# Kernel tuning notes

Measured on AMD Instinct MI355X. Metric: run time of the kernel, lower is better.

## Reference

```python
import jax, jax.numpy as jnp
import numpy as np

B = 65536
IN_F = 1024
OUT_F = 1024
N_ACT = 4  # len(activation_functions): tanh, sin, relu, sigmoid (cyclic over columns)


def setup_inputs() -> dict:
    key = jax.random.key(0)
    k1, k2 = jax.random.split(key)
    x = jax.random.normal(k1, (B, IN_F), dtype=jnp.float32)
    # xavier_uniform for weight [out, in]
    limit = float(np.sqrt(6.0 / (IN_F + OUT_F)))
    W = jax.random.uniform(k2, (OUT_F, IN_F), dtype=jnp.float32, minval=-limit, maxval=limit)
    b = jnp.zeros((OUT_F,), dtype=jnp.float32)
    return {"input": x, "W": W, "b": b}


def _apply_cyclic_acts(y):
    # column i gets activation (i % N_ACT); OUT_F % N_ACT == 0 so reshape to groups
    Bb, O = y.shape
    yg = y.reshape(Bb, O // N_ACT, N_ACT)
    out = jnp.stack([
        jnp.tanh(yg[..., 0]),
        jnp.sin(yg[..., 1]),
        jax.nn.relu(yg[..., 2]),
        jax.nn.sigmoid(yg[..., 3]),
    ], axis=-1)
    return out.reshape(Bb, O)


def reference(input, W, b) -> jnp.ndarray:
    y = jnp.einsum('bi,oi->bo', input, W) + b  # F.linear
    return _apply_cyclic_acts(y)
```

## Files before the change

### kernel.cpp

```cpp
#include <hip/hip_runtime.h>

constexpr int B_ROWS = 65536;
constexpr int IN_F   = 1024;
constexpr int OUT_F  = 1024;

constexpr int BDIM = 256;
constexpr int BM = 128, BN = 128, BK = 32;

typedef __bf16 bf16x8 __attribute__((ext_vector_type(8)));
typedef float  f32x4  __attribute__((ext_vector_type(4)));

__device__ __forceinline__ bf16x8 cvt8(f32x4 u0, f32x4 u1) {
    bf16x8 v;
    v[0] = (__bf16)u0[0]; v[1] = (__bf16)u0[1]; v[2] = (__bf16)u0[2]; v[3] = (__bf16)u0[3];
    v[4] = (__bf16)u1[0]; v[5] = (__bf16)u1[1]; v[6] = (__bf16)u1[2]; v[7] = (__bf16)u1[3];
    return v;
}

__device__ __forceinline__ void glds16(const __bf16* g, unsigned char* l) {
    __builtin_amdgcn_global_load_lds(
        (const __attribute__((address_space(1))) unsigned int*)(const void*)g,
        (__attribute__((address_space(3))) unsigned int*)(void*)l,
        16, 0, 0);
}

#define BAR_CNT() asm volatile("s_waitcnt vmcnt(4) lgkmcnt(0)\n\ts_barrier" ::: "memory")
#define BAR_ALL() asm volatile("s_waitcnt vmcnt(0) lgkmcnt(0)\n\ts_barrier" ::: "memory")

__global__ __launch_bounds__(256)
void w_to_bf16(const float* __restrict__ W, __bf16* __restrict__ Wb) {
    const int i = (blockIdx.x * 256 + threadIdx.x) * 8;
    f32x4 a = *(const f32x4*)(W + i);
    f32x4 b = *(const f32x4*)(W + i + 4);
    *(bf16x8*)(Wb + i) = cvt8(a, b);
}

__global__ __launch_bounds__(BDIM, 4)
void fused_linear_act(const float* __restrict__ X,
                      const __bf16* __restrict__ Wb,
                      const float* __restrict__ bias,
                      float* __restrict__ O)
{
    __shared__ __attribute__((aligned(16))) unsigned char lds[2 * 16384];

    const int bx  = blockIdx.x;
    const int xcd = bx & 7;
    const int idx = bx >> 3;
    const int nt  = idx & 7;
    const int mt  = xcd + 8 * (idx >> 3);
    const int m0 = mt * BM;
    const int n0 = nt * BN;

    const int tid  = threadIdx.x;
    const int lane = tid & 63;
    const int wave = tid >> 6;
    const int wm = (wave >> 1) * 64;
    const int wn = (wave & 1) * 64;
    const int lrow = lane & 15;
    const int quad = lane >> 4;

    const int srow = tid >> 2;
    const int sseg = tid & 3;

    f32x4 acc[4][4];
    #pragma unroll
    for (int i = 0; i < 4; ++i)
        #pragma unroll
        for (int j = 0; j < 4; ++j)
            acc[i][j] = (f32x4){0.f, 0.f, 0.f, 0.f};

    const float* xa = X + (size_t)(m0 + srow) * IN_F + sseg * 8;
    const float* xb = xa + (size_t)64 * IN_F;

    const __bf16* wsrc0 = Wb + (size_t)(n0 + 16 * wave + lrow) * IN_F + quad * 8;
    const __bf16* wsrc1 = wsrc0 + (size_t)64 * IN_F;
    unsigned char* ldsB0 = lds + 8192 + wave * 1024;
    unsigned char* ldsB1 = ldsB0 + 4096;

    unsigned char* wr = &lds[((srow >> 4) * 64 + sseg * 16 + (srow & 15)) * 16];
    const unsigned char* rdA = &lds[(wm >> 4) * 1024 + lane * 16];
    const unsigned char* rdB = &lds[8192 + (wn >> 4) * 1024 + lane * 16];

    f32x4 A00 = *(const f32x4*)(xa);
    f32x4 A01 = *(const f32x4*)(xa + 4);
    f32x4 A10 = *(const f32x4*)(xb);
    f32x4 A11 = *(const f32x4*)(xb + 4);
    glds16(wsrc0, ldsB0);
    glds16(wsrc1, ldsB1);
    __builtin_amdgcn_sched_barrier(0);

    int koffA = 0;
    int koffB = 0;

    auto stageA = [&](int buf) {
        unsigned char* w = wr + buf * 16384;
        *(bf16x8*)(w +    0) = cvt8(A00, A01);
        *(bf16x8*)(w + 4096) = cvt8(A10, A11);
        koffA = (koffA + BK) & (IN_F - 1);
        A00 = *(const f32x4*)(xa + koffA); A01 = *(const f32x4*)(xa + koffA + 4);
        A10 = *(const f32x4*)(xb + koffA); A11 = *(const f32x4*)(xb + koffA + 4);
    };
    auto stageB = [&](int buf) {
        koffB += BK;
        glds16(wsrc0 + koffB, ldsB0 + buf * 16384);
        glds16(wsrc1 + koffB, ldsB1 + buf * 16384);
        __builtin_amdgcn_sched_barrier(0);
    };
    auto compute = [&](int buf) {
        const unsigned char* ra = rdA + buf * 16384;
        const unsigned char* rb = rdB + buf * 16384;
        bf16x8 af[4], bfr[4];
        #pragma unroll
        for (int t = 0; t < 4; ++t) af[t]  = *(const bf16x8*)(ra + t * 1024);
        #pragma unroll
        for (int t = 0; t < 4; ++t) bfr[t] = *(const bf16x8*)(rb + t * 1024);
        #pragma unroll
        for (int i = 0; i < 4; ++i)
            #pragma unroll
            for (int j = 0; j < 4; ++j)
                acc[i][j] = __builtin_amdgcn_mfma_f32_16x16x32_bf16(af[i], bfr[j], acc[i][j], 0, 0, 0);
    };

    #pragma unroll 1
    for (int it = 0; it < IN_F / BK - 2; it += 2) {
        stageA(0); BAR_CNT(); stageB(1); compute(0);
        stageA(1); BAR_CNT(); stageB(0); compute(1);
    }
    stageA(0); BAR_CNT(); stageB(1); compute(0);
    stageA(1); BAR_ALL(); compute(1);

    const int s = lane & 3;
    const float kmul = (s == 0) ? -2.f : -1.f;
    const float aa   = (s == 0) ?  2.f :  1.f;
    const float cc   = (s == 0) ? -1.f :  0.f;
    const bool  is_sin  = (s == 1);
    const bool  is_relu = (s == 2);

    #pragma unroll
    for (int j = 0; j < 4; ++j) {
        const int gc = n0 + wn + j * 16 + lrow;
        const float bv = bias[gc];
        #pragma unroll
        for (int i = 0; i < 4; ++i) {
            const int gr0 = m0 + wm + i * 16 + quad * 4;
            float* op = O + (size_t)gr0 * OUT_F + gc;
            #pragma unroll
            for (int r = 0; r < 4; ++r) {
                const float y = acc[i][j][r] + bv;
                const float e = __expf(kmul * y);
                const float g = fmaf(aa, __builtin_amdgcn_rcpf(1.f + e), cc);
                const float sv = __sinf(y);
                const float rv = fmaxf(y, 0.f);
                const float res = is_sin ? sv : (is_relu ? rv : g);
                op[(size_t)r * OUT_F] = res;
            }
        }
    }
}

extern "C" void kernel_launch(void* const* d_in, const int* in_sizes, int n_in,
                              void* d_out, int out_size, void* d_ws, size_t ws_size,
                              hipStream_t stream) {
    const float* X = (const float*)d_in[0];
    const float* W = (const float*)d_in[1];
    const float* b = (const float*)d_in[2];
    float* O = (float*)d_out;
    __bf16* Wb = (__bf16*)d_ws;

    w_to_bf16<<<(OUT_F * IN_F) / (256 * 8), 256, 0, stream>>>(W, Wb);

    const int grid = (B_ROWS / BM) * (OUT_F / BN);
    fused_linear_act<<<grid, BDIM, 0, stream>>>(X, Wb, b, O);
}
```

Before: 654.8 us.

## Pre-convert activations to bf16 and triple-buffer async LDS loads for both operands

```diff
diff --git a/kernel.cpp b/kernel.cpp
--- a/kernel.cpp
+++ b/kernel.cpp
@@ -24,24 +24,27 @@
         16, 0, 0);
 }
 
-#define BAR_CNT() asm volatile("s_waitcnt vmcnt(4) lgkmcnt(0)\n\ts_barrier" ::: "memory")
-#define BAR_ALL() asm volatile("s_waitcnt vmcnt(0) lgkmcnt(0)\n\ts_barrier" ::: "memory")
+#define BARC() asm volatile("s_waitcnt vmcnt(4) lgkmcnt(0)\n\ts_barrier" ::: "memory")
+#define BAR0() asm volatile("s_waitcnt vmcnt(0) lgkmcnt(0)\n\ts_barrier" ::: "memory")
 
 __global__ __launch_bounds__(256)
-void w_to_bf16(const float* __restrict__ W, __bf16* __restrict__ Wb) {
-    const int i = (blockIdx.x * 256 + threadIdx.x) * 8;
-    f32x4 a = *(const f32x4*)(W + i);
-    f32x4 b = *(const f32x4*)(W + i + 4);
-    *(bf16x8*)(Wb + i) = cvt8(a, b);
-}
-
-__global__ __launch_bounds__(BDIM, 4)
-void fused_linear_act(const float* __restrict__ X,
+void cvt_bf16(const float* __restrict__ in, __bf16* __restrict__ out) {
+    const size_t i = ((size_t)blockIdx.x * 256 + threadIdx.x) * 16;
+    f32x4 a0 = *(const f32x4*)(in + i);
+    f32x4 a1 = *(const f32x4*)(in + i + 4);
+    f32x4 a2 = *(const f32x4*)(in + i + 8);
+    f32x4 a3 = *(const f32x4*)(in + i + 12);
+    *(bf16x8*)(out + i)     = cvt8(a0, a1);
+    *(bf16x8*)(out + i + 8) = cvt8(a2, a3);
+}
+
+__global__ __launch_bounds__(BDIM, 3)
+void fused_linear_act(const __bf16* __restrict__ Xb,
                       const __bf16* __restrict__ Wb,
                       const float* __restrict__ bias,
                       float* __restrict__ O)
 {
-    __shared__ __attribute__((aligned(16))) unsigned char lds[2 * 16384];
+    __shared__ __attribute__((aligned(16))) unsigned char lds[3 * 16384];
 
     const int bx  = blockIdx.x;
     const int xcd = bx & 7;
@@ -59,6 +62,116 @@
     const int lrow = lane & 15;
     const int quad = lane >> 4;
 
+    f32x4 acc[4][4];
+    #pragma unroll
+    for (int i = 0; i < 4; ++i)
+        #pragma unroll
+        for (int j = 0; j < 4; ++j)
+            acc[i][j] = (f32x4){0.f, 0.f, 0.f, 0.f};
+
+    const __bf16* asrc0 = Xb + (size_t)(m0 + 16 * wave + lrow) * IN_F + quad * 8;
+    const __bf16* asrc1 = asrc0 + (size_t)64 * IN_F;
+    const __bf16* bsrc0 = Wb + (size_t)(n0 + 16 * wave + lrow) * IN_F + quad * 8;
+    const __bf16* bsrc1 = bsrc0 + (size_t)64 * IN_F;
+    const int wlds = wave * 1024;
+
+    unsigned char* const buf0 = lds;
+    unsigned char* const buf1 = lds + 16384;
+    unsigned char* const buf2 = lds + 32768;
+
+    const int rdAoff = (wm >> 4) * 1024 + lane * 16;
+    const int rdBoff = 8192 + (wn >> 4) * 1024 + lane * 16;
+
+    auto stage = [&](int koff, unsigned char* base) {
+        glds16(asrc0 + koff, base + wlds);
+        glds16(asrc1 + koff, base + wlds + 4096);
+        glds16(bsrc0 + koff, base + 8192 + wlds);
+        glds16(bsrc1 + koff, base + 8192 + wlds + 4096);
+    };
+    auto compute = [&](const unsigned char* base) {
+        const unsigned char* ra = base + rdAoff;
+        const unsigned char* rb = base + rdBoff;
+        bf16x8 af[4], bfr[4];
+        #pragma unroll
+        for (int t = 0; t < 4; ++t) af[t]  = *(const bf16x8*)(ra + t * 1024);
+        #pragma unroll
+        for (int t = 0; t < 4; ++t) bfr[t] = *(const bf16x8*)(rb + t * 1024);
+        #pragma unroll
+        for (int i = 0; i < 4; ++i)
+            #pragma unroll
+            for (int j = 0; j < 4; ++j)
+                acc[i][j] = __builtin_amdgcn_mfma_f32_16x16x32_bf16(af[i], bfr[j], acc[i][j], 0, 0, 0);
+    };
+
+    stage(0,  buf0);
+    stage(32, buf1);
+
+    int koff = 64;
+    #pragma unroll 1
+    for (int it = 0; it < 10; ++it) {
+        BARC(); stage(koff, buf2); compute(buf0); koff += 32;
+        BARC(); stage(koff, buf0); compute(buf1); koff += 32;
+        BARC(); stage(koff, buf1); compute(buf2); koff += 32;
+    }
+    BARC(); compute(buf0);
+    BAR0(); compute(buf1);
+
+    const int s = lane & 3;
+    const float kmul = (s == 0) ? -2.f : -1.f;
+    const float aa   = (s == 0) ?  2.f :  1.f;
+    const float cc   = (s == 0) ? -1.f :  0.f;
+    const bool  is_sin  = (s == 1);
+    const bool  is_relu = (s == 2);
+
+    float bv[4];
+    #pragma unroll
+    for (int j = 0; j < 4; ++j) bv[j] = bias[n0 + wn + j * 16 + lrow];
+
+    #pragma unroll
+    for (int i = 0; i < 4; ++i) {
+        #pragma unroll
+        for (int r = 0; r < 4; ++r) {
+            const int gr = m0 + wm + i * 16 + quad * 4 + r;
+            float* op = O + (size_t)gr * OUT_F + n0 + wn + lrow;
+            #pragma unroll
+            for (int j = 0; j < 4; ++j) {
+                const float y = acc[i][j][r] + bv[j];
+                const float e = __expf(kmul * y);
+                const float g = fmaf(aa, __builtin_amdgcn_rcpf(1.f + e), cc);
+                const float sv = __sinf(y);
+                const float rv = fmaxf(y, 0.f);
+                const float res = is_sin ? sv : (is_relu ? rv : g);
+                op[j * 16] = res;
+            }
+        }
+    }
+}
+
+#define LDS_SYNC() asm volatile("s_waitcnt lgkmcnt(0)\n\ts_barrier" ::: "memory")
+#define BAR_CNT() asm volatile("s_waitcnt vmcnt(4) lgkmcnt(0)\n\ts_barrier" ::: "memory")
+#define BAR_ALL() asm volatile("s_waitcnt vmcnt(0) lgkmcnt(0)\n\ts_barrier" ::: "memory")
+
+__global__ __launch_bounds__(BDIM, 4)
+void fused_linear_act_f32a(const float* __restrict__ X,
+                           const __bf16* __restrict__ Wb,
+                           const float* __restrict__ bias,
+                           float* __restrict__ O)
+{
+    __shared__ __attribute__((aligned(16))) unsigned char lds[2 * 16384];
+    const int bx  = blockIdx.x;
+    const int xcd = bx & 7;
+    const int idx = bx >> 3;
+    const int nt  = idx & 7;
+    const int mt  = xcd + 8 * (idx >> 3);
+    const int m0 = mt * BM;
+    const int n0 = nt * BN;
+    const int tid  = threadIdx.x;
+    const int lane = tid & 63;
+    const int wave = tid >> 6;
+    const int wm = (wave >> 1) * 64;
+    const int wn = (wave & 1) * 64;
+    const int lrow = lane & 15;
+    const int quad = lane >> 4;
     const int srow = tid >> 2;
     const int sseg = tid & 3;
 
@@ -71,12 +184,10 @@
 
     const float* xa = X + (size_t)(m0 + srow) * IN_F + sseg * 8;
     const float* xb = xa + (size_t)64 * IN_F;
-
     const __bf16* wsrc0 = Wb + (size_t)(n0 + 16 * wave + lrow) * IN_F + quad * 8;
     const __bf16* wsrc1 = wsrc0 + (size_t)64 * IN_F;
     unsigned char* ldsB0 = lds + 8192 + wave * 1024;
     unsigned char* ldsB1 = ldsB0 + 4096;
-
     unsigned char* wr = &lds[((srow >> 4) * 64 + sseg * 16 + (srow & 15)) * 16];
     const unsigned char* rdA = &lds[(wm >> 4) * 1024 + lane * 16];
     const unsigned char* rdB = &lds[8192 + (wn >> 4) * 1024 + lane * 16];
@@ -89,9 +200,7 @@
     glds16(wsrc1, ldsB1);
     __builtin_amdgcn_sched_barrier(0);
 
-    int koffA = 0;
-    int koffB = 0;
-
+    int koffA = 0, koffB = 0;
     auto stageA = [&](int buf) {
         unsigned char* w = wr + buf * 16384;
         *(bf16x8*)(w +    0) = cvt8(A00, A01);
@@ -135,18 +244,17 @@
     const float cc   = (s == 0) ? -1.f :  0.f;
     const bool  is_sin  = (s == 1);
     const bool  is_relu = (s == 2);
-
     #pragma unroll
     for (int j = 0; j < 4; ++j) {
         const int gc = n0 + wn + j * 16 + lrow;
-        const float bv = bias[gc];
+        const float bvv = bias[gc];
         #pragma unroll
         for (int i = 0; i < 4; ++i) {
             const int gr0 = m0 + wm + i * 16 + quad * 4;
             float* op = O + (size_t)gr0 * OUT_F + gc;
             #pragma unroll
             for (int r = 0; r < 4; ++r) {
-                const float y = acc[i][j][r] + bv;
+                const float y = acc[i][j][r] + bvv;
                 const float e = __expf(kmul * y);
                 const float g = fmaf(aa, __builtin_amdgcn_rcpf(1.f + e), cc);
                 const float sv = __sinf(y);
@@ -165,10 +273,21 @@
     const float* W = (const float*)d_in[1];
     const float* b = (const float*)d_in[2];
     float* O = (float*)d_out;
-    __bf16* Wb = (__bf16*)d_ws;
-
-    w_to_bf16<<<(OUT_F * IN_F) / (256 * 8), 256, 0, stream>>>(W, Wb);
-
+
+    const size_t nX = (size_t)B_ROWS * IN_F;
+    const size_t nW = (size_t)OUT_F * IN_F;
+    const size_t need = (nX + nW) * sizeof(__bf16);
     const int grid = (B_ROWS / BM) * (OUT_F / BN);
-    fused_linear_act<<<grid, BDIM, 0, stream>>>(X, Wb, b, O);
-}
+
+    if (ws_size >= need) {
+        __bf16* Xb = (__bf16*)d_ws;
+        __bf16* Wb = Xb + nX;
+        cvt_bf16<<<(int)(nX / (256 * 16)), 256, 0, stream>>>(X, Xb);
+        cvt_bf16<<<(int)(nW / (256 * 16)), 256, 0, stream>>>(W, Wb);
+        fused_linear_act<<<grid, BDIM, 0, stream>>>(Xb, Wb, b, O);
+    } else {
+        __bf16* Wb = (__bf16*)d_ws;
+        cvt_bf16<<<(int)(nW / (256 * 16)), 256, 0, stream>>>(W, Wb);
+        fused_linear_act_f32a<<<grid, BDIM, 0, stream>>>(X, Wb, b, O);
+    }
+}
```

Measured after the change: 690.6 us. 1.05x slower.

## Enlarge GEMM tiles to 256x256x64 with 8 waves and interleaved LDS pipeline

Applied to the files above, without the earlier changes.

```diff
diff --git a/kernel.cpp b/kernel.cpp
--- a/kernel.cpp
+++ b/kernel.cpp
@@ -4,8 +4,8 @@
 constexpr int IN_F   = 1024;
 constexpr int OUT_F  = 1024;
 
-constexpr int BDIM = 256;
-constexpr int BM = 128, BN = 128, BK = 32;
+constexpr int BDIM = 512;
+constexpr int BM = 256, BN = 256, BK = 64;
 
 typedef __bf16 bf16x8 __attribute__((ext_vector_type(8)));
 typedef float  f32x4  __attribute__((ext_vector_type(4)));
@@ -24,110 +24,145 @@
         16, 0, 0);
 }
 
-#define BAR_CNT() asm volatile("s_waitcnt vmcnt(4) lgkmcnt(0)\n\ts_barrier" ::: "memory")
-#define BAR_ALL() asm volatile("s_waitcnt vmcnt(0) lgkmcnt(0)\n\ts_barrier" ::: "memory")
-
 __global__ __launch_bounds__(256)
 void w_to_bf16(const float* __restrict__ W, __bf16* __restrict__ Wb) {
-    const int i = (blockIdx.x * 256 + threadIdx.x) * 8;
-    f32x4 a = *(const f32x4*)(W + i);
-    f32x4 b = *(const f32x4*)(W + i + 4);
-    *(bf16x8*)(Wb + i) = cvt8(a, b);
-}
-
-__global__ __launch_bounds__(BDIM, 4)
+    const size_t i = ((size_t)blockIdx.x * 256 + threadIdx.x) * 16;
+    f32x4 a0 = *(const f32x4*)(W + i);
+    f32x4 a1 = *(const f32x4*)(W + i + 4);
+    f32x4 a2 = *(const f32x4*)(W + i + 8);
+    f32x4 a3 = *(const f32x4*)(W + i + 12);
+    *(bf16x8*)(Wb + i)     = cvt8(a0, a1);
+    *(bf16x8*)(Wb + i + 8) = cvt8(a2, a3);
+}
+
+
+__global__ __launch_bounds__(BDIM, 2)
 void fused_linear_act(const float* __restrict__ X,
                       const __bf16* __restrict__ Wb,
                       const float* __restrict__ bias,
                       float* __restrict__ O)
 {
-    __shared__ __attribute__((aligned(16))) unsigned char lds[2 * 16384];
+    __shared__ __attribute__((aligned(16))) unsigned char lds[2 * 65536];
 
     const int bx  = blockIdx.x;
     const int xcd = bx & 7;
     const int idx = bx >> 3;
-    const int nt  = idx & 7;
-    const int mt  = xcd + 8 * (idx >> 3);
+    const int nt  = idx & 3;
+    const int mt  = xcd + 8 * (idx >> 2);
     const int m0 = mt * BM;
     const int n0 = nt * BN;
 
     const int tid  = threadIdx.x;
     const int lane = tid & 63;
     const int wave = tid >> 6;
-    const int wm = (wave >> 1) * 64;
-    const int wn = (wave & 1) * 64;
+    const int wm2  = (wave >> 2) * 128;
+    const int wn2  = (wave & 3) * 64;
     const int lrow = lane & 15;
     const int quad = lane >> 4;
 
-    const int srow = tid >> 2;
-    const int sseg = tid & 3;
-
-    f32x4 acc[4][4];
+    const int arow = tid >> 1;
+    const int ah   = tid & 1;
+    const float* asrc = X + (size_t)(m0 + arow) * IN_F + ah * 32;
+    const int awr = ah * 16384 + (arow >> 4) * 1024 + (arow & 15) * 16;
+
+    const __bf16* bs0 = Wb + (size_t)(n0 + (wave & 3) * 64 + lrow) * IN_F
+                           + (wave >> 2) * 32 + quad * 8;
+    const __bf16* bs1 = bs0 + (size_t)16 * IN_F;
+    const __bf16* bs2 = bs0 + (size_t)32 * IN_F;
+    const __bf16* bs3 = bs0 + (size_t)48 * IN_F;
+    const int bdst = 32768 + (wave >> 2) * 16384 + (wave & 3) * 4096;
+
+    const int rdA = (wave >> 2) * 8192 + lane * 16;
+    const int rdB = 32768 + (wave & 3) * 4096 + lane * 16;
+
+    unsigned char* const b0 = lds;
+    unsigned char* const b1 = lds + 65536;
+
+    f32x4 acc[8][4];
     #pragma unroll
-    for (int i = 0; i < 4; ++i)
+    for (int i = 0; i < 8; ++i)
         #pragma unroll
         for (int j = 0; j < 4; ++j)
             acc[i][j] = (f32x4){0.f, 0.f, 0.f, 0.f};
 
-    const float* xa = X + (size_t)(m0 + srow) * IN_F + sseg * 8;
-    const float* xb = xa + (size_t)64 * IN_F;
-
-    const __bf16* wsrc0 = Wb + (size_t)(n0 + 16 * wave + lrow) * IN_F + quad * 8;
-    const __bf16* wsrc1 = wsrc0 + (size_t)64 * IN_F;
-    unsigned char* ldsB0 = lds + 8192 + wave * 1024;
-    unsigned char* ldsB1 = ldsB0 + 4096;
-
-    unsigned char* wr = &lds[((srow >> 4) * 64 + sseg * 16 + (srow & 15)) * 16];
-    const unsigned char* rdA = &lds[(wm >> 4) * 1024 + lane * 16];
-    const unsigned char* rdB = &lds[8192 + (wn >> 4) * 1024 + lane * 16];
-
-    f32x4 A00 = *(const f32x4*)(xa);
-    f32x4 A01 = *(const f32x4*)(xa + 4);
-    f32x4 A10 = *(const f32x4*)(xb);
-    f32x4 A11 = *(const f32x4*)(xb + 4);
-    glds16(wsrc0, ldsB0);
-    glds16(wsrc1, ldsB1);
-    __builtin_amdgcn_sched_barrier(0);
-
-    int koffA = 0;
-    int koffB = 0;
-
-    auto stageA = [&](int buf) {
-        unsigned char* w = wr + buf * 16384;
-        *(bf16x8*)(w +    0) = cvt8(A00, A01);
-        *(bf16x8*)(w + 4096) = cvt8(A10, A11);
-        koffA = (koffA + BK) & (IN_F - 1);
-        A00 = *(const f32x4*)(xa + koffA); A01 = *(const f32x4*)(xa + koffA + 4);
-        A10 = *(const f32x4*)(xb + koffA); A11 = *(const f32x4*)(xb + koffA + 4);
-    };
-    auto stageB = [&](int buf) {
-        koffB += BK;
-        glds16(wsrc0 + koffB, ldsB0 + buf * 16384);
-        glds16(wsrc1 + koffB, ldsB1 + buf * 16384);
-        __builtin_amdgcn_sched_barrier(0);
-    };
-    auto compute = [&](int buf) {
-        const unsigned char* ra = rdA + buf * 16384;
-        const unsigned char* rb = rdB + buf * 16384;
-        bf16x8 af[4], bfr[4];
-        #pragma unroll
-        for (int t = 0; t < 4; ++t) af[t]  = *(const bf16x8*)(ra + t * 1024);
-        #pragma unroll
-        for (int t = 0; t < 4; ++t) bfr[t] = *(const bf16x8*)(rb + t * 1024);
-        #pragma unroll
-        for (int i = 0; i < 4; ++i)
-            #pragma unroll
-            for (int j = 0; j < 4; ++j)
-                acc[i][j] = __builtin_amdgcn_mfma_f32_16x16x32_bf16(af[i], bfr[j], acc[i][j], 0, 0, 0);
-    };
+    f32x4 ar0, ar1, ar2, ar3, ar4, ar5, ar6, ar7;
+    bf16x8 aq0, aq1, aq2, aq3, bq0, bq1, bq2, bq3;
+
+#define ALOAD_LO(KA) do { \
+    ar0 = *(const f32x4*)(asrc + (KA));      ar1 = *(const f32x4*)(asrc + (KA) + 4);  \
+    ar2 = *(const f32x4*)(asrc + (KA) + 8);  ar3 = *(const f32x4*)(asrc + (KA) + 12); } while (0)
+#define ALOAD_HI(KA) do { \
+    ar4 = *(const f32x4*)(asrc + (KA) + 16); ar5 = *(const f32x4*)(asrc + (KA) + 20); \
+    ar6 = *(const f32x4*)(asrc + (KA) + 24); ar7 = *(const f32x4*)(asrc + (KA) + 28); } while (0)
+#define DSW(NXTB) do { unsigned char* _w = (NXTB) + awr; \
+    *(bf16x8*)(_w)       = cvt8(ar0, ar1); \
+    *(bf16x8*)(_w + 256) = cvt8(ar2, ar3); \
+    *(bf16x8*)(_w + 512) = cvt8(ar4, ar5); \
+    *(bf16x8*)(_w + 768) = cvt8(ar6, ar7); } while (0)
+#define GLDSB(NXTB, KB) do { unsigned char* _d = (NXTB) + bdst; \
+    glds16(bs0 + (KB), _d);        glds16(bs1 + (KB), _d + 1024); \
+    glds16(bs2 + (KB), _d + 2048); glds16(bs3 + (KB), _d + 3072); } while (0)
+#define READ_A(CURB, KS, MH) do { \
+    const unsigned char* _ra = (CURB) + rdA + (KS) * 16384 + (MH) * 4096; \
+    aq0 = *(const bf16x8*)(_ra);        aq1 = *(const bf16x8*)(_ra + 1024); \
+    aq2 = *(const bf16x8*)(_ra + 2048); aq3 = *(const bf16x8*)(_ra + 3072); } while (0)
+#define READ_B(CURB, KS) do { \
+    const unsigned char* _rb = (CURB) + rdB + (KS) * 16384; \
+    bq0 = *(const bf16x8*)(_rb);        bq1 = *(const bf16x8*)(_rb + 1024); \
+    bq2 = *(const bf16x8*)(_rb + 2048); bq3 = *(const bf16x8*)(_rb + 3072); } while (0)
+#define MFMA1(MH, I, J) acc[(MH)*4+(I)][(J)] = \
+    __builtin_amdgcn_mfma_f32_16x16x32_bf16(aq##I, bq##J, acc[(MH)*4+(I)][(J)], 0, 0, 0)
+#define MFMAQ(MH) do { __builtin_amdgcn_s_setprio(1); \
+    MFMA1(MH,0,0); MFMA1(MH,0,1); MFMA1(MH,0,2); MFMA1(MH,0,3); \
+    MFMA1(MH,1,0); MFMA1(MH,1,1); MFMA1(MH,1,2); MFMA1(MH,1,3); \
+    MFMA1(MH,2,0); MFMA1(MH,2,1); MFMA1(MH,2,2); MFMA1(MH,2,3); \
+    MFMA1(MH,3,0); MFMA1(MH,3,1); MFMA1(MH,3,2); MFMA1(MH,3,3); \
+    __builtin_amdgcn_s_setprio(0); } while (0)
+#define VM8    asm volatile("s_waitcnt vmcnt(8)" ::: "memory")
+#define VM0    asm volatile("s_waitcnt vmcnt(0)" ::: "memory")
+#define VMNONE ((void)0)
+
+#define ROUND(CURB, NXTB, DO_GLDS, KB, DO_DSW, DO_ALOAD, KA, VMW) do { \
+     \
+    if (DO_GLDS) GLDSB(NXTB, KB); \
+    READ_B(CURB, 0); READ_A(CURB, 0, 0); \
+    __builtin_amdgcn_s_barrier(); \
+    MFMAQ(0); \
+     \
+    if (DO_DSW) DSW(NXTB); \
+    if (DO_ALOAD) ALOAD_LO(KA); \
+    READ_A(CURB, 0, 1); \
+    __builtin_amdgcn_s_barrier(); \
+    MFMAQ(1); \
+     \
+    if (DO_ALOAD) ALOAD_HI(KA); \
+    READ_B(CURB, 1); READ_A(CURB, 1, 0); \
+    __builtin_amdgcn_s_barrier(); \
+    MFMAQ(0); \
+     \
+    READ_A(CURB, 1, 1); \
+    asm volatile("s_waitcnt lgkmcnt(0)" ::: "memory"); \
+    VMW; \
+    __builtin_amdgcn_s_barrier(); \
+    MFMAQ(1); \
+} while (0)
+
+    ALOAD_LO(0); ALOAD_HI(0);
+    GLDSB(b0, 0);
+    DSW(b0);
+    ALOAD_LO(64); ALOAD_HI(64);
+    asm volatile("s_waitcnt vmcnt(8) lgkmcnt(0)" ::: "memory");
+    __builtin_amdgcn_s_barrier();
 
     #pragma unroll 1
-    for (int it = 0; it < IN_F / BK - 2; it += 2) {
-        stageA(0); BAR_CNT(); stageB(1); compute(0);
-        stageA(1); BAR_CNT(); stageB(0); compute(1);
+    for (int t = 0; t < 14; t += 2) {
+        const int kb0 = (t + 1) * 64, ka0 = (t + 2) * 64;
+        ROUND(b0, b1, true, kb0, true, true, ka0, VM8);
+        const int kb1 = (t + 2) * 64, ka1 = (t + 3) * 64;
+        ROUND(b1, b0, true, kb1, true, true, ka1, VM8);
     }
-    stageA(0); BAR_CNT(); stageB(1); compute(0);
-    stageA(1); BAR_ALL(); compute(1);
+    ROUND(b0, b1, true, 15 * 64, true, false, 0, VM0);
+    ROUND(b1, b0, false, 0, false, false, 0, VMNONE);
 
     const int s = lane & 3;
     const float kmul = (s == 0) ? -2.f : -1.f;
@@ -136,23 +171,25 @@
     const bool  is_sin  = (s == 1);
     const bool  is_relu = (s == 2);
 
+    float bv[4];
     #pragma unroll
-    for (int j = 0; j < 4; ++j) {
-        const int gc = n0 + wn + j * 16 + lrow;
-        const float bv = bias[gc];
+    for (int fn = 0; fn < 4; ++fn) bv[fn] = bias[n0 + wn2 + fn * 16 + lrow];
+
+    #pragma unroll
+    for (int fm = 0; fm < 8; ++fm) {
         #pragma unroll
-        for (int i = 0; i < 4; ++i) {
-            const int gr0 = m0 + wm + i * 16 + quad * 4;
-            float* op = O + (size_t)gr0 * OUT_F + gc;
+        for (int r = 0; r < 4; ++r) {
+            const int gr = m0 + wm2 + fm * 16 + quad * 4 + r;
+            float* op = O + (size_t)gr * OUT_F + n0 + wn2 + lrow;
             #pragma unroll
-            for (int r = 0; r < 4; ++r) {
-                const float y = acc[i][j][r] + bv;
+            for (int fn = 0; fn < 4; ++fn) {
+                const float y = acc[fm][fn][r] + bv[fn];
                 const float e = __expf(kmul * y);
                 const float g = fmaf(aa, __builtin_amdgcn_rcpf(1.f + e), cc);
                 const float sv = __sinf(y);
                 const float rv = fmaxf(y, 0.f);
                 const float res = is_sin ? sv : (is_relu ? rv : g);
-                op[(size_t)r * OUT_F] = res;
+                op[fn * 16] = res;
             }
         }
     }
@@ -167,7 +204,8 @@
     float* O = (float*)d_out;
     __bf16* Wb = (__bf16*)d_ws;
 
-    w_to_bf16<<<(OUT_F * IN_F) / (256 * 8), 256, 0, stream>>>(W, Wb);
+    const size_t nW = (size_t)OUT_F * IN_F;
+    w_to_bf16<<<(int)(nW / (256 * 16)), 256, 0, stream>>>(W, Wb);
 
     const int grid = (B_ROWS / BM) * (OUT_F / BN);
     fused_linear_act<<<grid, BDIM, 0, stream>>>(X, Wb, b, O);
```

Result: faster. 598.0 us (-8.7%).
